# Kernel tuning notes

Hardware: AMD Instinct MI355X
Metric: run time of the kernel (lower is better)

Reference implementation:

```python
import jax, jax.numpy as jnp
import numpy as np

B, N, NC = 16, 128, 32          # batch, num_vectors, num_condition_vectors
H, A, DEG = 256, 64, 3          # hidden_dim, attention_dim, degree
SCALE = float(np.sqrt(H) ** DEG)  # weights_scale = sqrt(hidden_dim)^degree = 4096
# S3 non-identity permutations lifted to batch tensor axes (batch axis 0 fixed)
PERMS = [(0, 1, 3, 2), (0, 2, 1, 3), (0, 2, 3, 1), (0, 3, 1, 2), (0, 3, 2, 1)]


def setup_inputs() -> dict:
    key = jax.random.key(0)
    ks = jax.random.split(key, 6)
    inv = 1.0 / np.sqrt(H)
    return {
        "x": jax.random.normal(ks[0], (B, N, H), jnp.float32),
        "x_mask": jnp.ones((B, N, 1), jnp.float32),
        "condition": jax.random.normal(ks[1], (B, NC, H), jnp.float32),
        "condition_mask": jnp.ones((B, NC, 1), jnp.float32),
        "W1": (jax.random.normal(ks[2], (DEG, H, H), jnp.float32) * inv),
        "b1": jnp.zeros((DEG, H), jnp.float32),
        "Wc": (jax.random.normal(ks[3], (DEG, H, H), jnp.float32) * inv),
        "Wlin": (jax.random.normal(ks[4], (DEG, H, A), jnp.float32) * inv),
        "blin": jnp.zeros((DEG, A), jnp.float32),
    }


def reference(x, x_mask, condition, condition_mask, W1, b1, Wc, Wlin, blin):
    # masked mean-pool of condition vectors: [B, H]
    pooled = (condition * condition_mask).sum(1) / jnp.maximum(condition_mask.sum(1), 1.0)
    ys, dvs = [], []
    for d in range(DEG):  # small fixed loop over structurally distinct branches
        dv = pooled @ Wc[d]                                   # daughter vector [B, H]
        h = jax.nn.gelu(x @ W1[d] + b1[d] + dv[:, None, :])   # branch encoder [B, N, H]
        y = (h @ Wlin[d] + blin[d]) * x_mask                  # linear + mask  [B, N, A]
        ys.append(y)
        dvs.append(dv)
    # degree-3 multilinear contraction: 'xbi,ybi,zbi->bxyz' == 'bxi,byi,bzi->bxyz'
    base = jnp.einsum('bxi,byi,bzi->bxyz', ys[0], ys[1], ys[2]) / SCALE
    # symmetrize: add all non-identity permuted views (S3 minus identity)
    out = base
    for p in PERMS:
        out = out + jnp.transpose(base, p)
    return out, jnp.stack(dvs)  # ([B,N,N,N], [DEG,B,H])
```

## Files before the change

kernel.cpp:

```cpp
#include <hip/hip_runtime.h>
#include <hip/hip_bf16.h>
#include <math.h>
#include <string.h>

#define BB   16
#define NN   128
#define NCC  32
#define HH   256
#define AA   64
#define DEGN 3
#define BNR  (BB*NN)

typedef __bf16 bf16x8 __attribute__((ext_vector_type(8)));
typedef float  f32x16 __attribute__((ext_vector_type(16)));

__device__ __forceinline__ unsigned int pk2(float lo, float hi) {
    __hip_bfloat162 h2 = __float22bfloat162_rn(make_float2(lo, hi));
    unsigned int u;
    memcpy(&u, &h2, 4);
    return u;
}
__device__ __forceinline__ float2 unpk(unsigned int u) {
    return make_float2(__uint_as_float(u << 16),
                       __uint_as_float(u & 0xffff0000u));
}
__device__ __forceinline__ unsigned short bfbits(float f) {
    __hip_bfloat16 h = __float2bfloat16(f);
    unsigned short u;
    memcpy(&u, &h, 2);
    return u;
}

__global__ __launch_bounds__(256) void k_head(const float* __restrict__ cond,
                                              const float* __restrict__ cmask,
                                              const float* __restrict__ Wc,
                                              const float* __restrict__ W1,
                                              const float* __restrict__ Wlin,
                                              float* __restrict__ dv,
                                              float* __restrict__ dv_out,
                                              unsigned short* __restrict__ W1t,
                                              unsigned short* __restrict__ Wlt) {
    __shared__ float shm[32 * 33];
    const int bid = blockIdx.x, t = threadIdx.x;

    if (bid < 48) {
        const int d = bid >> 4, b = bid & 15;
        float s = 0.f, ms = 0.f;
        for (int c = 0; c < NCC; ++c) {
            float mk = cmask[b * NCC + c];
            s  += cond[(b * NCC + c) * HH + t] * mk;
            ms += mk;
        }
        shm[t] = s / fmaxf(ms, 1.0f);
        __syncthreads();
        const float* Wd = Wc + (size_t)d * HH * HH;
        float acc = 0.f;
        for (int k = 0; k < HH; ++k) acc += shm[k] * Wd[k * HH + t];
        int idx = (d * BB + b) * HH + t;
        dv[idx]     = acc;
        dv_out[idx] = acc;
    } else if (bid < 240) {
        const int q = bid - 48;
        const int d = q >> 6, r2 = q & 63, tk = r2 >> 3, tn = r2 & 7;
        float (*tile)[33] = (float (*)[33])shm;
        #pragma unroll
        for (int p = 0; p < 4; ++p) {
            int kr = p * 8 + (t >> 5), nr = t & 31;
            tile[kr][nr] = W1[((size_t)d * HH + tk * 32 + kr) * HH + tn * 32 + nr];
        }
        __syncthreads();
        #pragma unroll
        for (int p = 0; p < 4; ++p) {
            int nr = p * 8 + (t >> 5), kr = t & 31;
            W1t[((size_t)d * HH + tn * 32 + nr) * HH + tk * 32 + kr] =
                bfbits(tile[kr][nr]);
        }
    } else {
        const int q = bid - 240;
        const int d = q >> 4, r3 = q & 15, tk = r3 >> 1, ta = r3 & 1;
        float (*tile)[33] = (float (*)[33])shm;
        #pragma unroll
        for (int p = 0; p < 4; ++p) {
            int kr = p * 8 + (t >> 5), ar = t & 31;
            tile[kr][ar] = Wlin[((size_t)d * HH + tk * 32 + kr) * AA + ta * 32 + ar];
        }
        __syncthreads();
        #pragma unroll
        for (int p = 0; p < 4; ++p) {
            int ar = p * 8 + (t >> 5), kr = t & 31;
            Wlt[((size_t)d * AA + ta * 32 + ar) * HH + tk * 32 + kr] =
                bfbits(tile[kr][ar]);
        }
    }
}

__global__ __launch_bounds__(256) void k_mlp(const float* __restrict__ x,
                                             const float* __restrict__ xmask,
                                             const float* __restrict__ b1,
                                             const float* __restrict__ blin,
                                             const float* __restrict__ dv,
                                             const unsigned short* __restrict__ W1t,
                                             const unsigned short* __restrict__ Wlt,
                                             float* __restrict__ yv) {
    __shared__ __align__(16) char ldsA[32 * 512];
    __shared__ float ps[2][32][68];

    const int t = threadIdx.x;
    const int d = blockIdx.x >> 6, rt = blockIdx.x & 63;
    const int row0 = rt * 32;
    const int b = row0 >> 7;
    const int lane = t & 63, wid = t >> 6;
    const int rl5 = lane & 31, h2v = lane >> 5;

    #pragma unroll
    for (int it = 0; it < 8; ++it) {
        const int r = wid * 8 + it;
        const float4 v = *(const float4*)&x[(size_t)(row0 + r) * HH + lane * 4];
        uint2 u = make_uint2(pk2(v.x, v.y), pk2(v.z, v.w));
        *(uint2*)(ldsA + r * 512 + ((lane * 8) ^ ((r & 7) << 4))) = u;
    }
    __syncthreads();

    f32x16 acc1[2];
    #pragma unroll
    for (int nt = 0; nt < 2; ++nt)
        #pragma unroll
        for (int e = 0; e < 16; ++e) acc1[nt][e] = 0.f;

    #pragma unroll
    for (int ks = 0; ks < 16; ++ks) {
        bf16x8 af = *(const bf16x8*)(ldsA + rl5 * 512 +
                      ((ks * 32 + h2v * 16) ^ ((rl5 & 7) << 4)));
        #pragma unroll
        for (int nt = 0; nt < 2; ++nt) {
            const int n = wid * 64 + nt * 32 + rl5;
            bf16x8 bf = *(const bf16x8*)(W1t +
                          ((size_t)d * HH + n) * HH + ks * 16 + h2v * 8);
            acc1[nt] = __builtin_amdgcn_mfma_f32_32x32x16_bf16(af, bf, acc1[nt], 0, 0, 0);
        }
    }
    __syncthreads();

    #pragma unroll
    for (int nt = 0; nt < 2; ++nt) {
        const int col = wid * 64 + nt * 32 + rl5;
        const float add = b1[d * HH + col] + dv[(d * BB + b) * HH + col];
        #pragma unroll
        for (int e = 0; e < 16; ++e) {
            const int row = (e & 3) + 8 * (e >> 2) + 4 * h2v;
            float v = acc1[nt][e] + add;
            float u = 0.7978845608028654f * (v + 0.044715f * v * v * v);
            float g = 0.5f * v * (1.0f + tanhf(u));
            *(unsigned short*)(ldsA + row * 512 + ((col * 2) ^ ((row & 7) << 4))) =
                bfbits(g);
        }
    }
    __syncthreads();

    const int qc = wid >> 1, kh = wid & 1;
    f32x16 acc2;
    #pragma unroll
    for (int e = 0; e < 16; ++e) acc2[e] = 0.f;
    #pragma unroll
    for (int ks = 0; ks < 8; ++ks) {
        const int kk = kh * 8 + ks;
        bf16x8 af = *(const bf16x8*)(ldsA + rl5 * 512 +
                      ((kk * 32 + h2v * 16) ^ ((rl5 & 7) << 4)));
        bf16x8 bf = *(const bf16x8*)(Wlt +
                      ((size_t)d * AA + qc * 32 + rl5) * HH + kk * 16 + h2v * 8);
        acc2 = __builtin_amdgcn_mfma_f32_32x32x16_bf16(af, bf, acc2, 0, 0, 0);
    }
    #pragma unroll
    for (int e = 0; e < 16; ++e) {
        const int row = (e & 3) + 8 * (e >> 2) + 4 * h2v;
        ps[kh][row][qc * 32 + rl5] = acc2[e];
    }
    __syncthreads();

    #pragma unroll
    for (int j = 0; j < 8; ++j) {
        const int idx = t * 8 + j;
        const int row = idx >> 6, a = idx & 63;
        float v = ps[0][row][a] + ps[1][row][a] + blin[d * AA + a];
        v *= xmask[row0 + row];
        yv[((size_t)d * BNR + row0 + row) * AA + a] = v;
    }
}

__device__ __forceinline__ void lds_fence_barrier() {
    asm volatile("s_waitcnt lgkmcnt(0)" ::: "memory");
    __builtin_amdgcn_s_barrier();
    __builtin_amdgcn_sched_barrier(0);
}
__device__ __forceinline__ void lds_wave_wait() {
    asm volatile("s_waitcnt lgkmcnt(0)" ::: "memory");
    __builtin_amdgcn_sched_barrier(0);
}

#define LROW 128

__global__ __launch_bounds__(256, 2) void k_contract(const float* __restrict__ yv,
                                                     float* __restrict__ outp) {
    __shared__ __align__(16) char lds[5 * 128 * LROW];
    char* A1b = lds;
    char* A2b = lds + 1 * 128 * LROW;
    char* Y0b = lds + 2 * 128 * LROW;
    char* B1b = lds + 3 * 128 * LROW;
    char* B2b = lds + 4 * 128 * LROW;

    const int t  = threadIdx.x;
    const int b  = blockIdx.x >> 5;
    const int xg = blockIdx.x & 31;

    const float* y0p = yv + (size_t)(0 * BNR + b * NN) * AA;
    const float* y1p = yv + (size_t)(1 * BNR + b * NN) * AA;
    const float* y2p = yv + (size_t)(2 * BNR + b * NN) * AA;

    const int lane = t & 63;
    const int wid  = t >> 6;
    const int li   = lane & 31;
    const int rh   = lane >> 5;
    const int rl5  = lane & 31, h2v = lane >> 5;
    const int wy   = wid * 32;

    float s0v[4], s1v[4], s2v[4];
    #pragma unroll
    for (int xi = 0; xi < 4; ++xi) {
        const int xr = xg * 4 + xi;
        s0v[xi] = y0p[xr * AA + lane];
        s1v[xi] = y1p[xr * AA + lane];
        s2v[xi] = y2p[xr * AA + lane];
    }

    #pragma unroll
    for (int it = 0; it < 16; ++it) {
        const int r   = wid * 32 + it * 2 + rh;
        const int swz = (r & 7) << 4;
        const int off = r * LROW + ((4 * li) ^ swz);
        const float2 v0 = *(const float2*)&y0p[r * AA + 2 * li];
        const float2 v1 = *(const float2*)&y1p[r * AA + 2 * li];
        const float2 v2 = *(const float2*)&y2p[r * AA + 2 * li];
        *(unsigned int*)(Y0b + off) = pk2(v0.x, v0.y);
        *(unsigned int*)(B1b + off) = pk2(v2.x, v2.y);
        *(unsigned int*)(B2b + off) = pk2(v1.x, v1.y);
    }

    const float inv = 1.0f / 4096.0f;
    char* scr1 = A1b + wid * 4096;
    char* scr2 = A2b + wid * 4096;

    #pragma unroll
    for (int xi = 0; xi < 4; ++xi) {
        const int xr = xg * 4 + xi;
        const float s0a = __shfl(s0v[xi], 2 * li), s0b = __shfl(s0v[xi], 2 * li + 1);
        const float s1a = __shfl(s1v[xi], 2 * li), s1b = __shfl(s1v[xi], 2 * li + 1);
        const float s2a = __shfl(s2v[xi], 2 * li), s2b = __shfl(s2v[xi], 2 * li + 1);

        if (xi == 0) lds_fence_barrier();

        #pragma unroll
        for (int it = 0; it < 16; ++it) {
            const int r   = wid * 32 + it * 2 + rh;
            const int swz = (r & 7) << 4;
            const int off = r * LROW + ((4 * li) ^ swz);
            const float2 y0 = unpk(*(const unsigned int*)(Y0b + off));
            const float2 y1 = unpk(*(const unsigned int*)(B2b + off));
            *(unsigned int*)(A1b + off) =
                pk2(s0a * y1.x + s1a * y0.x, s0b * y1.y + s1b * y0.y);
            *(unsigned int*)(A2b + off) = pk2(s2a * y0.x, s2b * y0.y);
        }
        lds_fence_barrier();

        f32x16 acc[4];
        #pragma unroll
        for (int ni = 0; ni < 4; ++ni)
            #pragma unroll
            for (int e = 0; e < 16; ++e) acc[ni][e] = 0.f;

        #pragma unroll
        for (int p = 0; p < 4; ++p) {
            const char* Ua = (p == 0) ? A1b : (p == 1) ? B1b : (p == 2) ? A2b : B2b;
            const char* Va = (p == 0) ? B1b : (p == 1) ? A1b : (p == 2) ? B2b : A2b;
            #pragma unroll
            for (int ks = 0; ks < 4; ++ks) {
                const int arow = wy + rl5;
                bf16x8 af = *(const bf16x8*)(Ua + arow * LROW +
                              ((ks * 32 + h2v * 16) ^ ((arow & 7) << 4)));
                #pragma unroll
                for (int ni = 0; ni < 4; ++ni) {
                    const int brow = ni * 32 + rl5;
                    bf16x8 bf = *(const bf16x8*)(Va + brow * LROW +
                                  ((ks * 32 + h2v * 16) ^ ((brow & 7) << 4)));
                    acc[ni] = __builtin_amdgcn_mfma_f32_32x32x16_bf16(
                        af, bf, acc[ni], 0, 0, 0);
                }
            }
        }
        lds_fence_barrier();

        float* osl = outp + ((size_t)(b * NN + xr)) * (NN * NN);
        #pragma unroll
        for (int half = 0; half < 2; ++half) {
            #pragma unroll
            for (int ni = 0; ni < 4; ++ni) {
                const int colb = ni * 32 + rl5;
                #pragma unroll
                for (int e2 = 0; e2 < 8; ++e2) {
                    const int e    = half * 8 + e2;
                    const int rloc = (e2 & 3) + 8 * (e2 >> 2) + 4 * h2v;
                    char* reg = (e2 < 4) ? scr1 : scr2;
                    *(float*)(reg + ((rloc & 7) * 512) + colb * 4) =
                        acc[ni][e] * inv;
                }
            }
            lds_wave_wait();
            #pragma unroll
            for (int it2 = 0; it2 < 8; ++it2) {
                const int rloc = it2 * 2 + rh;
                const char* reg = (it2 < 4) ? scr1 : scr2;
                float4 v = *(const float4*)(reg + ((rloc & 7) * 512) + rl5 * 16);
                *(float4*)&osl[(size_t)(wy + half * 16 + rloc) * NN + rl5 * 4] = v;
            }
            lds_wave_wait();
        }
    }
}

extern "C" void kernel_launch(void* const* d_in, const int* in_sizes, int n_in,
                              void* d_out, int out_size, void* d_ws, size_t ws_size,
                              hipStream_t stream) {
    const float* x     = (const float*)d_in[0];
    const float* xmask = (const float*)d_in[1];
    const float* cond  = (const float*)d_in[2];
    const float* cmask = (const float*)d_in[3];
    const float* W1    = (const float*)d_in[4];
    const float* b1    = (const float*)d_in[5];
    const float* Wc    = (const float*)d_in[6];
    const float* Wlin  = (const float*)d_in[7];
    const float* blin  = (const float*)d_in[8];

    float* out = (float*)d_out;
    float* ws  = (float*)d_ws;

    float* dv  = ws;
    float* yv  = ws + 12288;
    unsigned short* W1t = (unsigned short*)((char*)d_ws + (size_t)(12288 + 393216) * 4);
    unsigned short* Wlt = W1t + (size_t)DEGN * HH * HH;
    float* dv_out = out + (size_t)BB * NN * NN * NN;

    k_head    <<<dim3(288), dim3(256), 0, stream>>>(cond, cmask, Wc, W1, Wlin,
                                                    dv, dv_out, W1t, Wlt);
    k_mlp     <<<dim3(DEGN * 64), dim3(256), 0, stream>>>(x, xmask, b1, blin, dv,
                                                          W1t, Wlt, yv);
    k_contract<<<dim3(BB * NN / 4), dim3(256), 0, stream>>>(yv, out);
}
```

Measured before the change: 57.15 us.

## Permute B-operand rows so MFMA accumulators store directly as float4

Remaps the B-operand row index to 4*lane+ni so each lane's four accumulator tiles hold four consecutive output columns. This removes the LDS scratch staging round-trip for the output. Each lane now writes float4 straight to global memory. The swizzle is changed to use bits 2-4 of the row so the new strided row access stays free of LDS bank conflicts.

Result: faster. 55.29 us (median of 3 runs) (-3.3%).

```diff
diff --git a/kernel.cpp b/kernel.cpp
--- a/kernel.cpp
+++ b/kernel.cpp
@@ -192,12 +192,9 @@
     __builtin_amdgcn_s_barrier();
     __builtin_amdgcn_sched_barrier(0);
 }
-__device__ __forceinline__ void lds_wave_wait() {
-    asm volatile("s_waitcnt lgkmcnt(0)" ::: "memory");
-    __builtin_amdgcn_sched_barrier(0);
-}
 
 #define LROW 128
+#define SWZ(r) ((((r) >> 2) & 7) << 4)
 
 __global__ __launch_bounds__(256, 2) void k_contract(const float* __restrict__ yv,
                                                      float* __restrict__ outp) {
@@ -235,8 +232,7 @@
     #pragma unroll
     for (int it = 0; it < 16; ++it) {
         const int r   = wid * 32 + it * 2 + rh;
-        const int swz = (r & 7) << 4;
-        const int off = r * LROW + ((4 * li) ^ swz);
+        const int off = r * LROW + ((4 * li) ^ SWZ(r));
         const float2 v0 = *(const float2*)&y0p[r * AA + 2 * li];
         const float2 v1 = *(const float2*)&y1p[r * AA + 2 * li];
         const float2 v2 = *(const float2*)&y2p[r * AA + 2 * li];
@@ -246,8 +242,6 @@
     }
 
     const float inv = 1.0f / 4096.0f;
-    char* scr1 = A1b + wid * 4096;
-    char* scr2 = A2b + wid * 4096;
 
     #pragma unroll
     for (int xi = 0; xi < 4; ++xi) {
@@ -261,8 +255,7 @@
         #pragma unroll
         for (int it = 0; it < 16; ++it) {
             const int r   = wid * 32 + it * 2 + rh;
-            const int swz = (r & 7) << 4;
-            const int off = r * LROW + ((4 * li) ^ swz);
+            const int off = r * LROW + ((4 * li) ^ SWZ(r));
             const float2 y0 = unpk(*(const unsigned int*)(Y0b + off));
             const float2 y1 = unpk(*(const unsigned int*)(B2b + off));
             *(unsigned int*)(A1b + off) =
@@ -285,12 +278,12 @@
             for (int ks = 0; ks < 4; ++ks) {
                 const int arow = wy + rl5;
                 bf16x8 af = *(const bf16x8*)(Ua + arow * LROW +
-                              ((ks * 32 + h2v * 16) ^ ((arow & 7) << 4)));
+                              ((ks * 32 + h2v * 16) ^ SWZ(arow)));
                 #pragma unroll
                 for (int ni = 0; ni < 4; ++ni) {
-                    const int brow = ni * 32 + rl5;
+                    const int brow = 4 * rl5 + ni;
                     bf16x8 bf = *(const bf16x8*)(Va + brow * LROW +
-                                  ((ks * 32 + h2v * 16) ^ ((brow & 7) << 4)));
+                                  ((ks * 32 + h2v * 16) ^ SWZ(brow)));
                     acc[ni] = __builtin_amdgcn_mfma_f32_32x32x16_bf16(
                         af, bf, acc[ni], 0, 0, 0);
                 }
@@ -300,28 +293,11 @@
 
         float* osl = outp + ((size_t)(b * NN + xr)) * (NN * NN);
         #pragma unroll
-        for (int half = 0; half < 2; ++half) {
-            #pragma unroll
-            for (int ni = 0; ni < 4; ++ni) {
-                const int colb = ni * 32 + rl5;
-                #pragma unroll
-                for (int e2 = 0; e2 < 8; ++e2) {
-                    const int e    = half * 8 + e2;
-                    const int rloc = (e2 & 3) + 8 * (e2 >> 2) + 4 * h2v;
-                    char* reg = (e2 < 4) ? scr1 : scr2;
-                    *(float*)(reg + ((rloc & 7) * 512) + colb * 4) =
-                        acc[ni][e] * inv;
-                }
-            }
-            lds_wave_wait();
-            #pragma unroll
-            for (int it2 = 0; it2 < 8; ++it2) {
-                const int rloc = it2 * 2 + rh;
-                const char* reg = (it2 < 4) ? scr1 : scr2;
-                float4 v = *(const float4*)(reg + ((rloc & 7) * 512) + rl5 * 16);
-                *(float4*)&osl[(size_t)(wy + half * 16 + rloc) * NN + rl5 * 4] = v;
-            }
-            lds_wave_wait();
+        for (int e = 0; e < 16; ++e) {
+            const int rowf = wy + (e & 3) + 8 * (e >> 2) + 4 * h2v;
+            float4 v = make_float4(acc[0][e] * inv, acc[1][e] * inv,
+                                   acc[2][e] * inv, acc[3][e] * inv);
+            *(float4*)&osl[(size_t)rowf * NN + 4 * rl5] = v;
         }
     }
 }
```
